# Kernel optimization log

Hardware: AMD Instinct MI355X
Metric: run time of the kernel (lower is better)

Reference implementation:

```python
import jax, jax.numpy as jnp
import numpy as np

B, S, H, NH, MAXLEN = 4, 1024, 2048, 16, 1024
HD = H // NH  # head_dim = 128

def setup_inputs() -> dict:
    key = jax.random.key(0)
    ks = jax.random.split(key, 16)
    def lin(i):
        # torch Linear default init ~ U(-1/sqrt(in), 1/sqrt(in)); store W as [in, out]
        bound = 1.0 / np.sqrt(H)
        W = jax.random.uniform(ks[i], (H, H), jnp.float32, -bound, bound)
        b = jax.random.uniform(ks[i + 1], (H,), jnp.float32, -bound, bound)
        return W, b
    Wq, bq = lin(0)
    Wk, bk = lin(2)
    Wv, bv = lin(4)
    Wu, bu = lin(6)
    Wf2, bf2 = lin(8)
    rel_table = jax.random.normal(ks[10], (2 * MAXLEN - 1, NH), jnp.float32)
    query = jax.random.normal(ks[11], (B, S, H), jnp.float32)
    key_t = jax.random.normal(ks[12], (B, S, H), jnp.float32)
    value = jax.random.normal(ks[13], (B, S, H), jnp.float32)
    # causal mask [B, Sq, Sk]
    attn_mask = jnp.broadcast_to(jnp.tril(jnp.ones((S, S), bool)), (B, S, S))
    return {"query": query, "key": key_t, "value": value, "attn_mask": attn_mask,
            "Wq": Wq, "bq": bq, "Wk": Wk, "bk": bk, "Wv": Wv, "bv": bv,
            "Wu": Wu, "bu": bu, "Wf2": Wf2, "bf2": bf2, "rel_table": rel_table}

def reference(query, key, value, attn_mask, Wq, bq, Wk, bk, Wv, bv, Wu, bu, Wf2, bf2, rel_table):
    silu = jax.nn.silu
    U = silu(query @ Wu + bu)                      # [B,S,H]
    Q = silu(query @ Wq + bq).reshape(B, S, NH, HD).transpose(0, 2, 1, 3)  # [B,NH,S,HD]
    K = silu(key @ Wk + bk).reshape(B, S, NH, HD).transpose(0, 2, 1, 3)
    V = silu(value @ Wv + bv).reshape(B, S, NH, HD).transpose(0, 2, 1, 3)
    scale = HD ** -0.5
    scores = jnp.einsum('bhqd,bhkd->bhqk', Q, K) * scale  # [B,NH,S,S]
    # relative position bias lookup (non-infer path)
    positions = jnp.arange(S)[:, None] - jnp.arange(S)[None, :]
    rel_idx = positions + MAXLEN - 1                       # [S,S]
    rel_bias = rel_table[rel_idx].transpose(2, 0, 1)[None]  # [1,NH,S,S]
    scores = scores + rel_bias
    attn = silu(scores)  # SiLU attention instead of softmax
    attn = jnp.where(attn_mask[:, None, :, :], attn, 0.0)
    out = jnp.einsum('bhqk,bhkd->bhqd', attn, V)           # [B,NH,S,HD]
    out = out.transpose(0, 2, 1, 3).reshape(B, S, H)
    gated = out * U
    return gated @ Wf2 + bf2
```

## Files before the change

### kernel.cpp

```cpp
#include <hip/hip_runtime.h>
#include <stdint.h>

#define HDIM 2048
#define SEQLEN 1024
#define NHEADS 16
#define HEADD 128

typedef unsigned short u16;
typedef unsigned int u32;
typedef __attribute__((ext_vector_type(8))) short bf16x8;
typedef __attribute__((ext_vector_type(8))) u16 u16x8;
typedef __attribute__((ext_vector_type(4))) u16 u16x4;
typedef __attribute__((ext_vector_type(4))) float f32x4;

__device__ __forceinline__ float bf2f(u16 u) {
    union { u32 i; float f; } v; v.i = ((u32)u) << 16; return v.f;
}
__device__ __forceinline__ u16 f2bf(float f) {
    union { float f; u32 i; } v; v.f = f;
    return (u16)((v.i + 0x7fffu + ((v.i >> 16) & 1u)) >> 16);
}
__device__ __forceinline__ u16 f2bf_t(float f) {
    union { float f; u32 i; } v; v.f = f; return (u16)(v.i >> 16);
}
__device__ __forceinline__ float silu_f(float x) {
    return x * __builtin_amdgcn_rcpf(1.f + __expf(-x));
}
__device__ __forceinline__ void glds16(const void* g, void* l) {
    __builtin_amdgcn_global_load_lds(
        (const __attribute__((address_space(1))) u32*)g,
        (__attribute__((address_space(3))) u32*)l, 16, 0, 0);
}

__global__ __launch_bounds__(256) void f32_to_bf16(const float* __restrict__ in,
                                                   u16* __restrict__ out, int n8) {
    int i = blockIdx.x * 256 + threadIdx.x;
    const int stride = gridDim.x * 256;
    for (; i < n8; i += stride) {
        f32x4 a = *(const f32x4*)&in[(size_t)i * 8];
        f32x4 b = *(const f32x4*)&in[(size_t)i * 8 + 4];
        u16x8 o;
#pragma unroll
        for (int j = 0; j < 4; ++j) { o[j] = f2bf(a[j]); o[4 + j] = f2bf(b[j]); }
        *(u16x8*)&out[(size_t)i * 8] = o;
    }
}

__global__ __launch_bounds__(256) void transpose_w(const float* __restrict__ W,
                                                   u16* __restrict__ WT) {
    __shared__ u16 T[64][76];
    const int r0 = blockIdx.y * 64;
    const int c0 = blockIdx.x * 64;
    const int t = threadIdx.x;
#pragma unroll
    for (int c = t; c < 1024; c += 256) {
        const int r = c >> 4, cc = (c & 15) << 2;
        f32x4 v = *(const f32x4*)&W[(size_t)(r0 + r) * HDIM + c0 + cc];
        u16x4 o;
#pragma unroll
        for (int j = 0; j < 4; ++j) o[j] = f2bf(v[j]);
        *(u16x4*)&T[r][cc] = o;
    }
    __syncthreads();
#pragma unroll
    for (int c = t; c < 512; c += 256) {
        const int n = c >> 3, kc = (c & 7) << 3;
        u16x8 v;
#pragma unroll
        for (int j = 0; j < 8; ++j) v[j] = T[kc + j][n];
        *(u16x8*)&WT[(size_t)(c0 + n) * HDIM + r0 + kc] = v;
    }
}

__global__ __launch_bounds__(256) void transpose_v(const u16* __restrict__ V,
                                                   u16* __restrict__ VT) {
    __shared__ u16 T[64][76];
    const int bh = blockIdx.y;
    const int st = (blockIdx.x & 15) * 64;
    const int dt = (blockIdx.x >> 4) * 64;
    const int b = bh >> 4, h = bh & 15;
    const int t = threadIdx.x;
#pragma unroll
    for (int c = t; c < 1024; c += 256) {
        const int s = c >> 4, d4 = (c & 15) << 2;
        *(u16x4*)&T[s][d4] =
            *(const u16x4*)&V[(size_t)(b * SEQLEN + st + s) * HDIM + h * HEADD + dt + d4];
    }
    __syncthreads();
#pragma unroll
    for (int c = t; c < 512; c += 256) {
        const int d = c >> 3, s8 = (c & 7) << 3;
        u16x8 v;
#pragma unroll
        for (int j = 0; j < 8; ++j) v[j] = T[s8 + j][d];
        *(u16x8*)&VT[((size_t)bh * HEADD + dt + d) * SEQLEN + st + s8] = v;
    }
}

__global__ __launch_bounds__(512, 2) void gemm256_8p(
    const u16* __restrict__ X,
    const u16* __restrict__ WTq, const u16* __restrict__ WTu,
    const float* __restrict__ bq, const float* __restrict__ bu,
    u16* __restrict__ Qo, u16* __restrict__ Uo)
{
    extern __shared__ u16 lds[];
    const int t = threadIdx.x;
    const int lane = t & 63, wid = t >> 6;
    const int l15 = lane & 15, l4 = lane >> 4;
    const int wr = wid >> 2, wn = wid & 3;

    const int bid = blockIdx.x;
    const int u = (bid & 7) * 32 + (bid >> 3);
    const int tm = u & 15, tn = u >> 4;
    const int m0 = tm * 256;
    const int n0 = tn * 256;
    const u16* WT = (n0 < 2048) ? WTq : WTu;
    const float* bias = (n0 < 2048) ? bq : bu;
    u16* outp = (n0 < 2048) ? Qo : Uo;
    const int nc0 = n0 & 2047;

    const int r64 = t >> 3;
    const int cse = (((t & 7) ^ (r64 & 7)) << 3);
    const u16* gA = X + (size_t)(m0 + r64) * HDIM + cse;
    const int rB0 = (r64 >> 5) * 64 + (r64 & 31);
    const u16* gB = WT + (size_t)(nc0 + rB0) * HDIM + cse;

    const int wbase = wid * 512;
    const int dstBw = (wid >> 2) * 4096 + (wid & 3) * 512;

    int offA[8][2], offB[4][2];
#pragma unroll
    for (int mf = 0; mf < 8; ++mf) {
        const int row = wr * 128 + mf * 16 + l15;
#pragma unroll
        for (int kk = 0; kk < 2; ++kk) {
            const int c = kk * 4 + l4;
            offA[mf][kk] = row * 64 + (((c) ^ (row & 7)) << 3);
        }
    }
#pragma unroll
    for (int nf = 0; nf < 4; ++nf) {
        const int row = wn * 64 + nf * 16 + l15;
#pragma unroll
        for (int kk = 0; kk < 2; ++kk) {
            const int c = kk * 4 + l4;
            offB[nf][kk] = 16384 + row * 64 + (((c) ^ (row & 7)) << 3);
        }
    }

#define SA(buf, rb, kt) glds16(gA + (size_t)(rb) * HDIM + (kt) * 64, \
                               lds + (buf) * 32768 + (rb) * 64 + wbase)
#define SB(buf, c, half, kt) glds16(gB + (size_t)((c) * 128 + (half) * 32) * HDIM + (kt) * 64, \
                               lds + (buf) * 32768 + 16384 + dstBw + (c) * 8192 + (half) * 2048)

    SA(0, 0, 0);    SA(0, 128, 0);
    SB(0, 0, 0, 0); SB(0, 1, 0, 0);
    SB(0, 0, 1, 0); SB(0, 1, 1, 0);
    SA(0, 64, 0);   SA(0, 192, 0);
    asm volatile("s_waitcnt vmcnt(4)" ::: "memory");
    __builtin_amdgcn_s_barrier();

    f32x4 acc[8][4] = {};
    int cur = 0;

#pragma unroll 1
    for (int kt = 0; kt < 32; ++kt) {
        const u16* pc = lds + cur * 32768;
        const int nb = cur ^ 1;
        const bool pf = (kt + 1 < 32);
        bf16x8 a[4][2], b0[2][2], b1[2][2];

#pragma unroll
        for (int mf = 0; mf < 4; ++mf)
#pragma unroll
            for (int kk = 0; kk < 2; ++kk)
                a[mf][kk] = *(const bf16x8*)(pc + offA[mf][kk]);
#pragma unroll
        for (int nf = 0; nf < 2; ++nf)
#pragma unroll
            for (int kk = 0; kk < 2; ++kk)
                b0[nf][kk] = *(const bf16x8*)(pc + offB[nf][kk]);
        if (pf) { SA(nb, 0, kt + 1); SA(nb, 128, kt + 1); }
        __builtin_amdgcn_s_barrier();
        asm volatile("s_waitcnt lgkmcnt(0)");
        __builtin_amdgcn_sched_barrier(0);
        __builtin_amdgcn_s_setprio(1);
#pragma unroll
        for (int mf = 0; mf < 4; ++mf)
#pragma unroll
            for (int nf = 0; nf < 2; ++nf)
#pragma unroll
                for (int kk = 0; kk < 2; ++kk)
                    acc[mf][nf] = __builtin_amdgcn_mfma_f32_16x16x32_bf16(
                        a[mf][kk], b0[nf][kk], acc[mf][nf], 0, 0, 0);
        __builtin_amdgcn_s_setprio(0);
        if (pf) { asm volatile("s_waitcnt vmcnt(4)" ::: "memory"); }
        else    { asm volatile("s_waitcnt vmcnt(2)" ::: "memory"); }
        __builtin_amdgcn_s_barrier();

#pragma unroll
        for (int nf = 0; nf < 2; ++nf)
#pragma unroll
            for (int kk = 0; kk < 2; ++kk)
                b1[nf][kk] = *(const bf16x8*)(pc + offB[2 + nf][kk]);
        if (pf) { SB(nb, 0, 0, kt + 1); SB(nb, 1, 0, kt + 1); }
        __builtin_amdgcn_s_barrier();
        asm volatile("s_waitcnt lgkmcnt(0)");
        __builtin_amdgcn_sched_barrier(0);
        __builtin_amdgcn_s_setprio(1);
#pragma unroll
        for (int mf = 0; mf < 4; ++mf)
#pragma unroll
            for (int nf = 0; nf < 2; ++nf)
#pragma unroll
                for (int kk = 0; kk < 2; ++kk)
                    acc[mf][2 + nf] = __builtin_amdgcn_mfma_f32_16x16x32_bf16(
                        a[mf][kk], b1[nf][kk], acc[mf][2 + nf], 0, 0, 0);
        __builtin_amdgcn_s_setprio(0);
        if (pf) { asm volatile("s_waitcnt vmcnt(4)" ::: "memory"); }
        else    { asm volatile("s_waitcnt vmcnt(0)" ::: "memory"); }
        __builtin_amdgcn_s_barrier();

#pragma unroll
        for (int mf = 0; mf < 4; ++mf)
#pragma unroll
            for (int kk = 0; kk < 2; ++kk)
                a[mf][kk] = *(const bf16x8*)(pc + offA[4 + mf][kk]);
        if (pf) {
            SB(nb, 0, 1, kt + 1); SB(nb, 1, 1, kt + 1);
            SA(nb, 64, kt + 1);   SA(nb, 192, kt + 1);
        }
        __builtin_amdgcn_s_barrier();
        asm volatile("s_waitcnt lgkmcnt(0)");
        __builtin_amdgcn_sched_barrier(0);
        __builtin_amdgcn_s_setprio(1);
#pragma unroll
        for (int mf = 0; mf < 4; ++mf)
#pragma unroll
            for (int nf = 0; nf < 2; ++nf)
#pragma unroll
                for (int kk = 0; kk < 2; ++kk)
                    acc[4 + mf][nf] = __builtin_amdgcn_mfma_f32_16x16x32_bf16(
                        a[mf][kk], b0[nf][kk], acc[4 + mf][nf], 0, 0, 0);
#pragma unroll
        for (int mf = 0; mf < 4; ++mf)
#pragma unroll
            for (int nf = 0; nf < 2; ++nf)
#pragma unroll
                for (int kk = 0; kk < 2; ++kk)
                    acc[4 + mf][2 + nf] = __builtin_amdgcn_mfma_f32_16x16x32_bf16(
                        a[mf][kk], b1[nf][kk], acc[4 + mf][2 + nf], 0, 0, 0);
        __builtin_amdgcn_s_setprio(0);
        if (pf) { asm volatile("s_waitcnt vmcnt(4)" ::: "memory"); }
        __builtin_amdgcn_s_barrier();
        cur ^= 1;
    }
#undef SA
#undef SB

    float bvv[4];
#pragma unroll
    for (int nf = 0; nf < 4; ++nf) bvv[nf] = bias[nc0 + wn * 64 + nf * 16 + l15];
#pragma unroll
    for (int mf = 0; mf < 8; ++mf) {
        const int mbase = m0 + wr * 128 + mf * 16 + (l4 << 2);
#pragma unroll
        for (int r = 0; r < 4; ++r) {
            u16* rowp = outp + (size_t)(mbase + r) * HDIM + nc0 + wn * 64 + l15;
#pragma unroll
            for (int nf = 0; nf < 4; ++nf)
                rowp[nf * 16] = f2bf(silu_f(acc[mf][nf][r] + bvv[nf]));
        }
    }
}

__global__ __launch_bounds__(256) void gemm128(
    const u16* __restrict__ X, const u16* __restrict__ WT,
    const float* __restrict__ bias, void* __restrict__ outp, const int mode)
{
    extern __shared__ u16 lds[];
    const int t = threadIdx.x;
    const int lane = t & 63, wid = t >> 6;
    const int l15 = lane & 15, l4 = lane >> 4;
    const int wr = wid >> 1, wn = wid & 1;

    const int bid = blockIdx.x;
    const int u = (bid & 7) * 64 + (bid >> 3);
    const int tm = u & 31, tn = u >> 5;
    const int m0 = tm * 128, n0 = tn * 128;

    const int ric = t >> 3;
    const int cse = (((t & 7) ^ (ric & 7)) << 3);
    const u16* gA = X  + (size_t)(m0 + ric) * HDIM + cse;
    const u16* gB = WT + (size_t)(n0 + ric) * HDIM + cse;

    u16* buf0 = lds;
    u16* buf1 = lds + 16384;
    const int wbase = wid * 512;

    int offA[4][2], offB[4][2];
#pragma unroll
    for (int i = 0; i < 4; ++i) {
        const int row = wr * 64 + i * 16 + l15;
#pragma unroll
        for (int kk = 0; kk < 2; ++kk)
            offA[i][kk] = ((row * 128 + kk * 64 + l4 * 16) ^ ((row & 7) << 4)) >> 1;
    }
#pragma unroll
    for (int j = 0; j < 4; ++j) {
        const int row = wn * 64 + j * 16 + l15;
#pragma unroll
        for (int kk = 0; kk < 2; ++kk)
            offB[j][kk] = 8192 + ((((row * 128 + kk * 64 + l4 * 16) ^ ((row & 7) << 4))) >> 1);
    }

#define STAGE_A(buf, c, kt) glds16(gA + (size_t)(c) * 32 * HDIM + (kt) * 64, (buf) + (c) * 2048 + wbase)
#define STAGE_B(buf, c, kt) glds16(gB + (size_t)(c) * 32 * HDIM + (kt) * 64, (buf) + 8192 + (c) * 2048 + wbase)

    STAGE_B(buf0, 0, 0); STAGE_B(buf0, 1, 0); STAGE_B(buf0, 2, 0); STAGE_B(buf0, 3, 0);
    STAGE_A(buf0, 0, 0); STAGE_A(buf0, 1, 0); STAGE_A(buf0, 2, 0); STAGE_A(buf0, 3, 0);
    STAGE_B(buf1, 0, 1); STAGE_B(buf1, 1, 1); STAGE_B(buf1, 2, 1); STAGE_B(buf1, 3, 1);
    STAGE_A(buf1, 0, 1); STAGE_A(buf1, 2, 1);
    asm volatile("s_waitcnt vmcnt(6)" ::: "memory");
    __builtin_amdgcn_s_barrier();

    f32x4 acc[4][4] = {};
    u16* pc = buf0;
    u16* pn = buf1;

#pragma unroll 1
    for (int tt = 0; tt < 32; ++tt) {
        bf16x8 bfr[4][2], afr[2][2];
#pragma unroll
        for (int j = 0; j < 4; ++j)
#pragma unroll
            for (int kk = 0; kk < 2; ++kk)
                bfr[j][kk] = *(const bf16x8*)(pc + offB[j][kk]);
#pragma unroll
        for (int i = 0; i < 2; ++i)
#pragma unroll
            for (int kk = 0; kk < 2; ++kk)
                afr[i][kk] = *(const bf16x8*)(pc + offA[i][kk]);
        if (tt + 1 < 32) { STAGE_A(pn, 1, tt + 1); STAGE_A(pn, 3, tt + 1); }
        __builtin_amdgcn_s_barrier();
        asm volatile("s_waitcnt lgkmcnt(0)");
        __builtin_amdgcn_sched_barrier(0);
        __builtin_amdgcn_s_setprio(1);
#pragma unroll
        for (int i = 0; i < 2; ++i)
#pragma unroll
            for (int j = 0; j < 4; ++j)
#pragma unroll
                for (int kk = 0; kk < 2; ++kk)
                    acc[i][j] = __builtin_amdgcn_mfma_f32_16x16x32_bf16(
                        afr[i][kk], bfr[j][kk], acc[i][j], 0, 0, 0);
        __builtin_amdgcn_s_setprio(0);
        __builtin_amdgcn_s_barrier();

#pragma unroll
        for (int i = 0; i < 2; ++i)
#pragma unroll
            for (int kk = 0; kk < 2; ++kk)
                afr[i][kk] = *(const bf16x8*)(pc + offA[2 + i][kk]);
        if (tt + 2 < 32) {
            STAGE_B(pc, 0, tt + 2); STAGE_B(pc, 1, tt + 2);
            STAGE_B(pc, 2, tt + 2); STAGE_B(pc, 3, tt + 2);
            STAGE_A(pc, 0, tt + 2); STAGE_A(pc, 2, tt + 2);
        }
        __builtin_amdgcn_s_barrier();
        asm volatile("s_waitcnt lgkmcnt(0)");
        __builtin_amdgcn_sched_barrier(0);
        __builtin_amdgcn_s_setprio(1);
#pragma unroll
        for (int i = 0; i < 2; ++i)
#pragma unroll
            for (int j = 0; j < 4; ++j)
#pragma unroll
                for (int kk = 0; kk < 2; ++kk)
                    acc[2 + i][j] = __builtin_amdgcn_mfma_f32_16x16x32_bf16(
                        afr[i][kk], bfr[j][kk], acc[2 + i][j], 0, 0, 0);
        __builtin_amdgcn_s_setprio(0);
        if (tt + 2 < 32)      { asm volatile("s_waitcnt vmcnt(6)" ::: "memory"); }
        else if (tt + 1 < 32) { asm volatile("s_waitcnt vmcnt(0)" ::: "memory"); }
        __builtin_amdgcn_s_barrier();
        u16* tmp = pc; pc = pn; pn = tmp;
    }
#undef STAGE_A
#undef STAGE_B

    float bvv[4];
#pragma unroll
    for (int j = 0; j < 4; ++j) bvv[j] = bias[n0 + wn * 64 + j * 16 + l15];
#pragma unroll
    for (int i = 0; i < 4; ++i) {
        const int mbase = m0 + wr * 64 + i * 16 + (l4 << 2);
#pragma unroll
        for (int r = 0; r < 4; ++r) {
            const size_t rowoff = (size_t)(mbase + r) * HDIM + n0 + wn * 64 + l15;
#pragma unroll
            for (int j = 0; j < 4; ++j) {
                const float v = acc[i][j][r] + bvv[j];
                if (mode == 0)
                    ((u16*)outp)[rowoff + j * 16] = f2bf(silu_f(v));
                else
                    ((float*)outp)[rowoff + j * 16] = v;
            }
        }
    }
}

__global__ __launch_bounds__(512) void attn_fused(
    const u16* __restrict__ Qb, const u16* __restrict__ Kb,
    const u16* __restrict__ VTg, const u16* __restrict__ Ub,
    const float* __restrict__ rel, u16* __restrict__ G)
{
    extern __shared__ u16 alds[];
    u16* Ps = alds + 24576;
    float* relh = (float*)(alds + 33792);

    const int idx = blockIdx.x;
    const int bh8 = idx & 7;
    const int j = (idx >> 3) & 7;
    const int bhhi = idx >> 6;
    const int bh = bhhi * 8 + bh8;
    const int b = bh >> 4, h = bh & 15;
    const int qS0 = j * 64;
    const int qL0 = (15 - j) * 64;
    const int nkt = 16 - j;
    const int t = threadIdx.x, lane = t & 63, w = t >> 6;
    const int wq = w & 3;
    const bool isL = (w < 4);
    const int l15 = lane & 15, l4 = lane >> 4, l3 = lane >> 3;
    const size_t rowbase = (size_t)b * SEQLEN;
    const int col0 = h * HEADD;
    const float scale = 0.088388347648318447f;

    for (int i = t; i < 1024; i += 512) relh[i] = rel[(size_t)(1023 + i) * NHEADS + h];

    const u16* gK0 = Kb + (rowbase + w * 8 + l4) * HDIM + col0 + ((lane & 15) ^ l4) * 8;
    const u16* gK1 = Kb + (rowbase + w * 8 + 4 + l4) * HDIM + col0 + ((lane & 15) ^ (l4 + 4)) * 8;
    const u16* gV0 = VTg + ((size_t)bh * HEADD + w * 16 + l3) * SEQLEN + ((lane & 7) ^ l3) * 8;
    const u16* gV1 = VTg + ((size_t)bh * HEADD + w * 16 + 8 + l3) * SEQLEN + ((lane & 7) ^ l3) * 8;

    const int q0 = (isL ? qL0 : qS0) + wq * 16;
    bf16x8 aq[4];
#pragma unroll
    for (int dc = 0; dc < 4; ++dc)
        aq[dc] = *(const bf16x8*)&Qb[(rowbase + q0 + l15) * HDIM + col0 + dc * 32 + (l4 << 3)];

    f32x4 oacc[8] = {};
    const int prB = (isL ? 0 : 64) + wq * 16;

#define STAGE_K(kt) do {                                                        \
    const size_t ko_ = (size_t)(kt) * 64 * HDIM;                                \
    glds16(gK0 + ko_, alds + w * 1024);                                         \
    glds16(gK1 + ko_, alds + w * 1024 + 512);                                   \
} while (0)
#define STAGE_V(kt, bsel) do {                                                  \
    u16* vb_ = alds + 8192 + ((bsel) ? 8192 : 0);                               \
    const size_t ko_ = (size_t)(kt) * 64;                                       \
    glds16(gV0 + ko_, vb_ + w * 1024);                                          \
    glds16(gV1 + ko_, vb_ + w * 1024 + 512);                                    \
} while (0)

    STAGE_K(0); STAGE_V(0, 0);
    asm volatile("s_waitcnt vmcnt(0)" ::: "memory");
    __builtin_amdgcn_s_barrier();

    int cur = 0;
#pragma unroll 1
    for (int kt = 0; kt < nkt; ++kt) {
        const int k0 = kt * 64;
        const bool act = isL || (kt <= j);
        const bool diag = isL ? (kt == nkt - 1) : (kt == j);
        if (kt + 1 < nkt) STAGE_V(kt + 1, cur ^ 1);
        const u16* kb = alds;
        const u16* vb = alds + 8192 + (cur ? 8192 : 0);

        if (act) {
#pragma unroll
            for (int kf = 0; kf < 4; ++kf) {
                const int krow = kf * 16 + l15;
                f32x4 s = {};
                __builtin_amdgcn_s_setprio(1);
#pragma unroll
                for (int dc = 0; dc < 4; ++dc) {
                    bf16x8 bk = *(const bf16x8*)&kb[krow * 128 + (((dc * 4 + l4) ^ (krow & 7)) << 3)];
                    s = __builtin_amdgcn_mfma_f32_16x16x32_bf16(aq[dc], bk, s, 0, 0, 0);
                }
                __builtin_amdgcn_s_setprio(0);
                const int kabs = k0 + krow;
                const int pr = prB + (l4 << 2);
                if (diag) {
#pragma unroll
                    for (int r = 0; r < 4; ++r) {
                        const int qabs = q0 + (l4 << 2) + r;
                        float v = 0.f;
                        if (kabs <= qabs) v = silu_f(fmaf(s[r], scale, relh[qabs - kabs]));
                        Ps[(pr + r) * 72 + kf * 16 + l15] = f2bf_t(v);
                    }
                } else {
#pragma unroll
                    for (int r = 0; r < 4; ++r) {
                        const int qabs = q0 + (l4 << 2) + r;
                        const float v = silu_f(fmaf(s[r], scale, relh[qabs - kabs]));
                        Ps[(pr + r) * 72 + kf * 16 + l15] = f2bf_t(v);
                    }
                }
            }
        }
        asm volatile("s_waitcnt lgkmcnt(0)" ::: "memory");
        __builtin_amdgcn_s_barrier();
        if (kt + 1 < nkt) STAGE_K(kt + 1);

        if (act) {
            bf16x8 ap[2];
#pragma unroll
            for (int kc = 0; kc < 2; ++kc)
                ap[kc] = *(const bf16x8*)&Ps[(prB + l15) * 72 + kc * 32 + (l4 << 3)];
            __builtin_amdgcn_s_setprio(1);
#pragma unroll
            for (int df = 0; df < 8; ++df) {
                const int vrow = df * 16 + l15;
#pragma unroll
                for (int kc = 0; kc < 2; ++kc) {
                    bf16x8 bv = *(const bf16x8*)&vb[vrow * 64 + (((kc * 4 + l4) ^ (vrow & 7)) << 3)];
                    oacc[df] = __builtin_amdgcn_mfma_f32_16x16x32_bf16(ap[kc], bv, oacc[df], 0, 0, 0);
                }
            }
            __builtin_amdgcn_s_setprio(0);
        }
        asm volatile("s_waitcnt vmcnt(0) lgkmcnt(0)" ::: "memory");
        __builtin_amdgcn_s_barrier();
        cur ^= 1;
    }
#undef STAGE_K
#undef STAGE_V

#pragma unroll
    for (int r = 0; r < 4; ++r) {
        const int qr = q0 + (l4 << 2) + r;
        const size_t row = (rowbase + qr) * HDIM + col0 + l15;
#pragma unroll
        for (int df = 0; df < 8; ++df)
            G[row + df * 16] = f2bf(oacc[df][r] * bf2f(Ub[row + df * 16]));
    }
}

extern "C" void kernel_launch(void* const* d_in, const int* in_sizes, int n_in,
                              void* d_out, int out_size, void* d_ws, size_t ws_size,
                              hipStream_t stream) {
    const float* query = (const float*)d_in[0];
    const float* key_  = (const float*)d_in[1];
    const float* value = (const float*)d_in[2];
    const float* Wq  = (const float*)d_in[4];  const float* bq  = (const float*)d_in[5];
    const float* Wk  = (const float*)d_in[6];  const float* bk  = (const float*)d_in[7];
    const float* Wv  = (const float*)d_in[8];  const float* bv  = (const float*)d_in[9];
    const float* Wu  = (const float*)d_in[10]; const float* bu  = (const float*)d_in[11];
    const float* Wf2 = (const float*)d_in[12]; const float* bf2 = (const float*)d_in[13];
    const float* rel = (const float*)d_in[14];

    char* ws = (char*)d_ws;
    const size_t WBYTES = (size_t)HDIM * HDIM * 2;
    const size_t ABYTES = (size_t)4096 * HDIM * 2;
    u16* WTa  = (u16*)ws;
    u16* Xbf  = (u16*)(ws + WBYTES);
    u16* Qbuf = (u16*)(ws + WBYTES + 1 * ABYTES);
    u16* Kbuf = (u16*)(ws + WBYTES + 2 * ABYTES);
    u16* Vbuf = (u16*)(ws + WBYTES + 3 * ABYTES);
    u16* Ubuf = (u16*)(ws + WBYTES + 4 * ABYTES);
    u16* WTb  = Vbuf;
    u16* Gbuf = Qbuf;
    u16* VTg  = Xbf;

    dim3 tpb(256);
    dim3 tgrid(32, 32);
    dim3 vgrid(32, 64);
    const int n8 = 4096 * HDIM / 8;
    const size_t GLDS  = 65536;
    const size_t G8LDS = 131072;
    const size_t ALDS  = 71680;

    f32_to_bf16<<<2048, tpb, 0, stream>>>(query, Xbf, n8);
    transpose_w<<<tgrid, tpb, 0, stream>>>(Wq, WTa);
    transpose_w<<<tgrid, tpb, 0, stream>>>(Wu, WTb);
    gemm256_8p<<<256, 512, G8LDS, stream>>>(Xbf, WTa, WTb, bq, bu, Qbuf, Ubuf);
    transpose_w<<<tgrid, tpb, 0, stream>>>(Wk, WTa);
    f32_to_bf16<<<2048, tpb, 0, stream>>>(key_, Xbf, n8);
    gemm128<<<512, tpb, GLDS, stream>>>(Xbf, WTa, bk, Kbuf, 0);
    transpose_w<<<tgrid, tpb, 0, stream>>>(Wv, WTa);
    f32_to_bf16<<<2048, tpb, 0, stream>>>(value, Xbf, n8);
    gemm128<<<512, tpb, GLDS, stream>>>(Xbf, WTa, bv, Vbuf, 0);
    transpose_v<<<vgrid, tpb, 0, stream>>>(Vbuf, VTg);
    attn_fused<<<512, 512, ALDS, stream>>>(Qbuf, Kbuf, VTg, Ubuf, rel, Gbuf);
    transpose_w<<<tgrid, tpb, 0, stream>>>(Wf2, WTa);
    gemm128<<<512, tpb, GLDS, stream>>>(Gbuf, WTa, bf2, d_out, 1);
}
```

Baseline: 310.9 us.

## Fuse V transpose into V-projection GEMM epilogue and restage 256-tile GEMM loop

Adds a mode 2 epilogue to gemm128 that applies bias and SiLU, stages the output tile transposed in LDS, and writes it directly in the [bh, d, s] layout the attention kernel expects. This removes the separate transpose_v kernel and its extra round trip of the V activation through global memory. The 256x256 Q/U GEMM main loop is also reorganised from three sub-stages to two: all four B fragments are loaded at once and the prefetch issue and vmcnt waits are rebalanced. This raises register pressure in that kernel and changes how prefetch latency is hidden.

Result: faster. 299.7 us (-3.6%).

```diff
diff --git a/kernel.cpp b/kernel.cpp
--- a/kernel.cpp
+++ b/kernel.cpp
@@ -69,31 +69,6 @@
 #pragma unroll
         for (int j = 0; j < 8; ++j) v[j] = T[kc + j][n];
         *(u16x8*)&WT[(size_t)(c0 + n) * HDIM + r0 + kc] = v;
-    }
-}
-
-__global__ __launch_bounds__(256) void transpose_v(const u16* __restrict__ V,
-                                                   u16* __restrict__ VT) {
-    __shared__ u16 T[64][76];
-    const int bh = blockIdx.y;
-    const int st = (blockIdx.x & 15) * 64;
-    const int dt = (blockIdx.x >> 4) * 64;
-    const int b = bh >> 4, h = bh & 15;
-    const int t = threadIdx.x;
-#pragma unroll
-    for (int c = t; c < 1024; c += 256) {
-        const int s = c >> 4, d4 = (c & 15) << 2;
-        *(u16x4*)&T[s][d4] =
-            *(const u16x4*)&V[(size_t)(b * SEQLEN + st + s) * HDIM + h * HEADD + dt + d4];
-    }
-    __syncthreads();
-#pragma unroll
-    for (int c = t; c < 512; c += 256) {
-        const int d = c >> 3, s8 = (c & 7) << 3;
-        u16x8 v;
-#pragma unroll
-        for (int j = 0; j < 8; ++j) v[j] = T[s8 + j][d];
-        *(u16x8*)&VT[((size_t)bh * HEADD + dt + d) * SEQLEN + st + s8] = v;
     }
 }
 
@@ -157,7 +132,7 @@
     SB(0, 0, 0, 0); SB(0, 1, 0, 0);
     SB(0, 0, 1, 0); SB(0, 1, 1, 0);
     SA(0, 64, 0);   SA(0, 192, 0);
-    asm volatile("s_waitcnt vmcnt(4)" ::: "memory");
+    asm volatile("s_waitcnt vmcnt(2)" ::: "memory");
     __builtin_amdgcn_s_barrier();
 
     f32x4 acc[8][4] = {};
@@ -168,7 +143,7 @@
         const u16* pc = lds + cur * 32768;
         const int nb = cur ^ 1;
         const bool pf = (kt + 1 < 32);
-        bf16x8 a[4][2], b0[2][2], b1[2][2];
+        bf16x8 a[4][2], b[4][2];
 
 #pragma unroll
         for (int mf = 0; mf < 4; ++mf)
@@ -176,11 +151,12 @@
             for (int kk = 0; kk < 2; ++kk)
                 a[mf][kk] = *(const bf16x8*)(pc + offA[mf][kk]);
 #pragma unroll
-        for (int nf = 0; nf < 2; ++nf)
+        for (int nf = 0; nf < 4; ++nf)
 #pragma unroll
             for (int kk = 0; kk < 2; ++kk)
-                b0[nf][kk] = *(const bf16x8*)(pc + offB[nf][kk]);
-        if (pf) { SA(nb, 0, kt + 1); SA(nb, 128, kt + 1); }
+                b[nf][kk] = *(const bf16x8*)(pc + offB[nf][kk]);
+        if (pf) { SA(nb, 0, kt + 1); SA(nb, 128, kt + 1);
+                  SB(nb, 0, 0, kt + 1); SB(nb, 1, 0, kt + 1); }
         __builtin_amdgcn_s_barrier();
         asm volatile("s_waitcnt lgkmcnt(0)");
         __builtin_amdgcn_sched_barrier(0);
@@ -188,22 +164,23 @@
 #pragma unroll
         for (int mf = 0; mf < 4; ++mf)
 #pragma unroll
-            for (int nf = 0; nf < 2; ++nf)
+            for (int nf = 0; nf < 4; ++nf)
 #pragma unroll
                 for (int kk = 0; kk < 2; ++kk)
                     acc[mf][nf] = __builtin_amdgcn_mfma_f32_16x16x32_bf16(
-                        a[mf][kk], b0[nf][kk], acc[mf][nf], 0, 0, 0);
+                        a[mf][kk], b[nf][kk], acc[mf][nf], 0, 0, 0);
         __builtin_amdgcn_s_setprio(0);
         if (pf) { asm volatile("s_waitcnt vmcnt(4)" ::: "memory"); }
-        else    { asm volatile("s_waitcnt vmcnt(2)" ::: "memory"); }
-        __builtin_amdgcn_s_barrier();
-
-#pragma unroll
-        for (int nf = 0; nf < 2; ++nf)
+        else    { asm volatile("s_waitcnt vmcnt(0)" ::: "memory"); }
+        __builtin_amdgcn_s_barrier();
+
+#pragma unroll
+        for (int mf = 0; mf < 4; ++mf)
 #pragma unroll
             for (int kk = 0; kk < 2; ++kk)
-                b1[nf][kk] = *(const bf16x8*)(pc + offB[2 + nf][kk]);
-        if (pf) { SB(nb, 0, 0, kt + 1); SB(nb, 1, 0, kt + 1); }
+                a[mf][kk] = *(const bf16x8*)(pc + offA[4 + mf][kk]);
+        if (pf) { SB(nb, 0, 1, kt + 1); SB(nb, 1, 1, kt + 1);
+                  SA(nb, 64, kt + 1);   SA(nb, 192, kt + 1); }
         __builtin_amdgcn_s_barrier();
         asm volatile("s_waitcnt lgkmcnt(0)");
         __builtin_amdgcn_sched_barrier(0);
@@ -211,47 +188,13 @@
 #pragma unroll
         for (int mf = 0; mf < 4; ++mf)
 #pragma unroll
-            for (int nf = 0; nf < 2; ++nf)
-#pragma unroll
-                for (int kk = 0; kk < 2; ++kk)
-                    acc[mf][2 + nf] = __builtin_amdgcn_mfma_f32_16x16x32_bf16(
-                        a[mf][kk], b1[nf][kk], acc[mf][2 + nf], 0, 0, 0);
-        __builtin_amdgcn_s_setprio(0);
-        if (pf) { asm volatile("s_waitcnt vmcnt(4)" ::: "memory"); }
-        else    { asm volatile("s_waitcnt vmcnt(0)" ::: "memory"); }
-        __builtin_amdgcn_s_barrier();
-
-#pragma unroll
-        for (int mf = 0; mf < 4; ++mf)
-#pragma unroll
-            for (int kk = 0; kk < 2; ++kk)
-                a[mf][kk] = *(const bf16x8*)(pc + offA[4 + mf][kk]);
-        if (pf) {
-            SB(nb, 0, 1, kt + 1); SB(nb, 1, 1, kt + 1);
-            SA(nb, 64, kt + 1);   SA(nb, 192, kt + 1);
-        }
-        __builtin_amdgcn_s_barrier();
-        asm volatile("s_waitcnt lgkmcnt(0)");
-        __builtin_amdgcn_sched_barrier(0);
-        __builtin_amdgcn_s_setprio(1);
-#pragma unroll
-        for (int mf = 0; mf < 4; ++mf)
-#pragma unroll
-            for (int nf = 0; nf < 2; ++nf)
+            for (int nf = 0; nf < 4; ++nf)
 #pragma unroll
                 for (int kk = 0; kk < 2; ++kk)
                     acc[4 + mf][nf] = __builtin_amdgcn_mfma_f32_16x16x32_bf16(
-                        a[mf][kk], b0[nf][kk], acc[4 + mf][nf], 0, 0, 0);
-#pragma unroll
-        for (int mf = 0; mf < 4; ++mf)
-#pragma unroll
-            for (int nf = 0; nf < 2; ++nf)
-#pragma unroll
-                for (int kk = 0; kk < 2; ++kk)
-                    acc[4 + mf][2 + nf] = __builtin_amdgcn_mfma_f32_16x16x32_bf16(
-                        a[mf][kk], b1[nf][kk], acc[4 + mf][2 + nf], 0, 0, 0);
+                        a[mf][kk], b[nf][kk], acc[4 + mf][nf], 0, 0, 0);
         __builtin_amdgcn_s_setprio(0);
-        if (pf) { asm volatile("s_waitcnt vmcnt(4)" ::: "memory"); }
+        if (pf) { asm volatile("s_waitcnt vmcnt(2)" ::: "memory"); }
         __builtin_amdgcn_s_barrier();
         cur ^= 1;
     }
@@ -391,6 +334,35 @@
     float bvv[4];
 #pragma unroll
     for (int j = 0; j < 4; ++j) bvv[j] = bias[n0 + wn * 64 + j * 16 + l15];
+
+    if (mode == 2) {
+        u16* Tv = lds;
+        __syncthreads();
+#pragma unroll
+        for (int i = 0; i < 4; ++i)
+#pragma unroll
+            for (int r = 0; r < 4; ++r) {
+                const int s = wr * 64 + i * 16 + (l4 << 2) + r;
+#pragma unroll
+                for (int j = 0; j < 4; ++j) {
+                    const int d = wn * 64 + j * 16 + l15;
+                    Tv[d * 136 + s] = f2bf(silu_f(acc[i][j][r] + bvv[j]));
+                }
+            }
+        __syncthreads();
+        const int bh = (m0 >> 10) * 16 + tn;
+        const int s0 = m0 & 1023;
+        u16* vt = (u16*)outp;
+#pragma unroll
+        for (int r8 = 0; r8 < 8; ++r8) {
+            const int d = (t >> 4) + r8 * 16;
+            const int s = (t & 15) * 8;
+            u16x8 v = *(const u16x8*)&Tv[d * 136 + s];
+            *(u16x8*)&vt[((size_t)bh * HEADD + d) * SEQLEN + s0 + s] = v;
+        }
+        return;
+    }
+
 #pragma unroll
     for (int i = 0; i < 4; ++i) {
         const int mbase = m0 + wr * 64 + i * 16 + (l4 << 2);
@@ -567,15 +539,13 @@
     u16* Xbf  = (u16*)(ws + WBYTES);
     u16* Qbuf = (u16*)(ws + WBYTES + 1 * ABYTES);
     u16* Kbuf = (u16*)(ws + WBYTES + 2 * ABYTES);
-    u16* Vbuf = (u16*)(ws + WBYTES + 3 * ABYTES);
+    u16* VTg  = (u16*)(ws + WBYTES + 3 * ABYTES);
     u16* Ubuf = (u16*)(ws + WBYTES + 4 * ABYTES);
-    u16* WTb  = Vbuf;
+    u16* WTb  = VTg;
     u16* Gbuf = Qbuf;
-    u16* VTg  = Xbf;
 
     dim3 tpb(256);
     dim3 tgrid(32, 32);
-    dim3 vgrid(32, 64);
     const int n8 = 4096 * HDIM / 8;
     const size_t GLDS  = 65536;
     const size_t G8LDS = 131072;
@@ -590,8 +560,7 @@
     gemm128<<<512, tpb, GLDS, stream>>>(Xbf, WTa, bk, Kbuf, 0);
     transpose_w<<<tgrid, tpb, 0, stream>>>(Wv, WTa);
     f32_to_bf16<<<2048, tpb, 0, stream>>>(value, Xbf, n8);
-    gemm128<<<512, tpb, GLDS, stream>>>(Xbf, WTa, bv, Vbuf, 0);
-    transpose_v<<<vgrid, tpb, 0, stream>>>(Vbuf, VTg);
+    gemm128<<<512, tpb, GLDS, stream>>>(Xbf, WTa, bv, VTg, 2);
     attn_fused<<<512, 512, ALDS, stream>>>(Qbuf, Kbuf, VTg, Ubuf, rel, Gbuf);
     transpose_w<<<tgrid, tpb, 0, stream>>>(Wf2, WTa);
     gemm128<<<512, tpb, GLDS, stream>>>(Gbuf, WTa, bf2, d_out, 1);
```
